# Kernel tuning notes

Hardware: AMD Instinct MI355X
Metric: run time of the kernel (lower is better)

The kernel has to match this reference:

```python
import jax, jax.numpy as jnp
import numpy as np


def setup_inputs() -> dict:
    key = jax.random.key(0)
    k1, k2, k3 = jax.random.split(key, 3)
    b, c, h, w = 4, 64, 64, 64
    content = jax.random.normal(k1, (b, c, h, w), dtype=jnp.float32)
    content_s = jax.random.normal(k2, (b, c, h, w), dtype=jnp.float32)
    style = jax.random.normal(k3, (b, c, h, w), dtype=jnp.float32)
    return {"content": content, "content_s": content_s, "style": style}


def reference(content, content_s, style):
    b, c, h, w = content.shape
    hw = h * w
    Fc = content.reshape(b, c, hw)      # [b, c, HW]
    Fs = content_s.reshape(b, c, hw)    # [b, c, HW]
    Fst = style.reshape(b, c, hw)       # [b, c, HW]
    # S[b, q, k] = sum_c Fc[b, c, q] * Fs[b, c, k]  (Fc transposed as in torch)
    S = jnp.einsum('bcq,bck->bqk', Fc, Fs)
    S = jax.nn.softmax(S, axis=-1)
    # O = style @ S^T : O[b, c, q] = sum_k Fst[b, c, k] * S[b, q, k]
    O = jnp.einsum('bck,bqk->bcq', Fst, S).reshape(b, c, h, w)
    return jnp.concatenate((content, O), axis=1)
```

## Files before the change

kernel.cpp:

```cpp
#include <hip/hip_runtime.h>
#include <math.h>


#define Bb 4
#define Cc 64
#define HWs 4096
#define SPLITS 4
#define TILES_PER_SPLIT 16
#define RLOG2E 1.44269504088896340736f

typedef _Float16 half8 __attribute__((ext_vector_type(8)));
typedef _Float16 half4 __attribute__((ext_vector_type(4)));
typedef float floatx4 __attribute__((ext_vector_type(4)));

__global__ __launch_bounds__(256) void prep_k(const float* __restrict__ content,
                                              const float* __restrict__ Fs,
                                              const float* __restrict__ Fst,
                                              float* __restrict__ out,
                                              _Float16* __restrict__ Kt,
                                              _Float16* __restrict__ Vt) {
    const int bid = blockIdx.x;
    const int t = threadIdx.x;
    if (bid < 1024) {
        int i4 = bid * 256 + t;
        const float4* c4 = (const float4*)content;
        const float4* v4 = (const float4*)Fst;
        float4* o4 = (float4*)out;
        int b = i4 >> 16, rem = i4 & 65535;
        o4[(size_t)b * 131072 + rem] = c4[i4];
        float4 v = v4[i4];
        half4 h;
        h[0] = (_Float16)v.x; h[1] = (_Float16)v.y;
        h[2] = (_Float16)v.z; h[3] = (_Float16)v.w;
        *(half4*)(Vt + (size_t)i4 * 4) = h;
    } else {
        __shared__ _Float16 T[16][72];
        int e = bid - 1024;
        int b = e >> 8;
        int hw0 = (e & 255) * 16;
        const float* sb = Fs + (size_t)b * Cc * HWs;
        {
            int c = t >> 2, x4 = (t & 3) * 4;
            float4 v = *(const float4*)(sb + (size_t)c * HWs + hw0 + x4);
            T[x4 + 0][c] = (_Float16)v.x;
            T[x4 + 1][c] = (_Float16)v.y;
            T[x4 + 2][c] = (_Float16)v.z;
            T[x4 + 3][c] = (_Float16)v.w;
        }
        __syncthreads();
        if (t < 128) {
            int row = t >> 3, g = t & 7;
            _Float16* db = Kt + (size_t)b * HWs * Cc;
            *(half8*)(db + (size_t)(hw0 + row) * Cc + g * 8) = *(half8*)&T[row][g * 8];
        }
    }
}

__global__ __launch_bounds__(256, 2) void attn_k(const float* __restrict__ Fc,
                                                 const _Float16* __restrict__ Kt,
                                                 const _Float16* __restrict__ Vt,
                                                 _Float16* __restrict__ Opart,
                                                 float2* __restrict__ ml) {
    const int tid  = threadIdx.x;
    const int w    = tid >> 6;
    const int lane = tid & 63;
    const int quad = lane >> 4;
    const int l15  = lane & 15;
    const int qg = blockIdx.x & 31;
    const int b  = (blockIdx.x >> 5) & 3;
    const int s  = blockIdx.x >> 7;
    const int k0base = s * TILES_PER_SPLIT * 64;
    const int qA = qg * 128 + w * 32 + l15;
    const int qB = qA + 16;

    __shared__ _Float16 Kl[2][64 * 64];
    __shared__ _Float16 Vl[2][64 * 64];
    __shared__ _Float16 Ps[4][32][72];

    const float*    Fcb = Fc + (size_t)b * Cc * HWs;
    const _Float16* Kb  = Kt + (size_t)b * HWs * Cc;
    const _Float16* Vb  = Vt + (size_t)b * Cc * HWs;

    const bool isK  = tid < 128;
    const int  sl   = tid & 127;
    const int  srow = sl >> 3;
    const int  sjg  = sl & 7;
    const int  ssw  = (sjg ^ (srow & 7)) * 8;

    half8 qf[2][2];
    #pragma unroll
    for (int j = 0; j < 8; ++j) {
        qf[0][0][j] = (_Float16)(Fcb[(size_t)(quad * 8 + j) * HWs + qA] * RLOG2E);
        qf[0][1][j] = (_Float16)(Fcb[(size_t)(32 + quad * 8 + j) * HWs + qA] * RLOG2E);
        qf[1][0][j] = (_Float16)(Fcb[(size_t)(quad * 8 + j) * HWs + qB] * RLOG2E);
        qf[1][1][j] = (_Float16)(Fcb[(size_t)(32 + quad * 8 + j) * HWs + qB] * RLOG2E);
    }

    half8 st[4];
    auto stage_load = [&](int kt) {
        int kk0 = k0base + kt * 64;
        #pragma unroll
        for (int i = 0; i < 4; ++i) {
            int row = srow + 16 * i;
            if (isK) st[i] = *(const half8*)(Kb + (size_t)(kk0 + row) * 64 + sjg * 8);
            else     st[i] = *(const half8*)(Vb + (size_t)row * HWs + kk0 + sjg * 8);
        }
    };
    auto stage_write = [&](int p) {
        #pragma unroll
        for (int i = 0; i < 4; ++i) {
            int row = srow + 16 * i;
            if (isK) *(half8*)&Kl[p][row * 64 + ssw] = st[i];
            else     *(half8*)&Vl[p][row * 64 + ssw] = st[i];
        }
    };

    floatx4 acc[2][4];
    #pragma unroll
    for (int g = 0; g < 2; ++g)
        #pragma unroll
        for (int m = 0; m < 4; ++m) acc[g][m] = (floatx4)(0.0f);
    float m_run[2] = {-INFINITY, -INFINITY};
    float lsum[2] = {0.0f, 0.0f};

    stage_load(0);
    stage_write(0);
    stage_load(1);
    __syncthreads();

    const int swl = (l15 & 7);
    for (int kt = 0; kt < TILES_PER_SPLIT; ++kt) {
        const int p = kt & 1;
        if (kt + 1 < TILES_PER_SPLIT) stage_write(p ^ 1);
        if (kt + 2 < TILES_PER_SPLIT) stage_load(kt + 2);

        half8 ka[4][2];
        #pragma unroll
        for (int m = 0; m < 4; ++m)
            #pragma unroll
            for (int cs = 0; cs < 2; ++cs)
                ka[m][cs] = *(const half8*)&Kl[p][(m * 16 + l15) * 64 + (((cs * 4 + quad) ^ swl) * 8)];

        floatx4 sv[2][4];
        #pragma unroll
        for (int m = 0; m < 4; ++m) {
            #pragma unroll
            for (int g = 0; g < 2; ++g) {
                sv[g][m] = __builtin_amdgcn_mfma_f32_16x16x32_f16(ka[m][0], qf[g][0], (floatx4)(0.0f), 0, 0, 0);
                sv[g][m] = __builtin_amdgcn_mfma_f32_16x16x32_f16(ka[m][1], qf[g][1], sv[g][m], 0, 0, 0);
            }
        }

        half8 va[4][2];
        #pragma unroll
        for (int m = 0; m < 4; ++m)
            #pragma unroll
            for (int ks = 0; ks < 2; ++ks)
                va[m][ks] = *(const half8*)&Vl[p][(m * 16 + l15) * 64 + (((ks * 4 + quad) ^ swl) * 8)];

        half8 pb[2][2];
        #pragma unroll
        for (int g = 0; g < 2; ++g) {
            float mx = -INFINITY;
            #pragma unroll
            for (int m = 0; m < 4; ++m)
                #pragma unroll
                for (int r = 0; r < 4; ++r) mx = fmaxf(mx, sv[g][m][r]);
            mx = fmaxf(mx, __shfl_xor(mx, 16));
            mx = fmaxf(mx, __shfl_xor(mx, 32));
            float m_new = fmaxf(m_run[g], mx);
            float alpha = exp2f(m_run[g] - m_new);
            m_run[g] = m_new;
            float part = 0.0f;
            #pragma unroll
            for (int m = 0; m < 4; ++m)
                #pragma unroll
                for (int r = 0; r < 4; ++r) {
                    float e = exp2f(sv[g][m][r] - m_new);
                    sv[g][m][r] = e;
                    part += e;
                }
            lsum[g] = lsum[g] * alpha + part;
            #pragma unroll
            for (int m = 0; m < 4; ++m)
                #pragma unroll
                for (int r = 0; r < 4; ++r) acc[g][m][r] *= alpha;

            #pragma unroll
            for (int m = 0; m < 4; ++m) {
                half4 pp;
                pp[0] = (_Float16)sv[g][m][0]; pp[1] = (_Float16)sv[g][m][1];
                pp[2] = (_Float16)sv[g][m][2]; pp[3] = (_Float16)sv[g][m][3];
                *(half4*)&Ps[w][g * 16 + l15][m * 16 + quad * 4] = pp;
            }
            pb[g][0] = *(half8*)&Ps[w][g * 16 + l15][quad * 8];
            pb[g][1] = *(half8*)&Ps[w][g * 16 + l15][32 + quad * 8];
        }

        #pragma unroll
        for (int m = 0; m < 4; ++m)
            #pragma unroll
            for (int g = 0; g < 2; ++g) {
                acc[g][m] = __builtin_amdgcn_mfma_f32_16x16x32_f16(va[m][0], pb[g][0], acc[g][m], 0, 0, 0);
                acc[g][m] = __builtin_amdgcn_mfma_f32_16x16x32_f16(va[m][1], pb[g][1], acc[g][m], 0, 0, 0);
            }

        __syncthreads();
    }

    _Float16* op = Opart + (((size_t)s * Bb + b) * Cc) * HWs;
    #pragma unroll
    for (int g = 0; g < 2; ++g) {
        lsum[g] += __shfl_xor(lsum[g], 16);
        lsum[g] += __shfl_xor(lsum[g], 32);
        int q = (g == 0) ? qA : qB;
        #pragma unroll
        for (int m = 0; m < 4; ++m)
            #pragma unroll
            for (int r = 0; r < 4; ++r) {
                int c = m * 16 + quad * 4 + r;
                op[(size_t)c * HWs + q] = (_Float16)acc[g][m][r];
            }
        if (quad == 0)
            ml[((size_t)b * HWs + q) * SPLITS + s] = make_float2(m_run[g], lsum[g]);
    }
}

__global__ __launch_bounds__(256) void combine_k(const _Float16* __restrict__ Opart,
                                                 const float2* __restrict__ ml,
                                                 float* __restrict__ out) {
    int idx = blockIdx.x * 256 + threadIdx.x;
    int q = idx & 4095;
    int c = (idx >> 12) & 63;
    int b = idx >> 18;
    const float2* mlp = ml + ((size_t)b * HWs + q) * SPLITS;
    float2 mls[SPLITS];
    #pragma unroll
    for (int s = 0; s < SPLITS; ++s) mls[s] = mlp[s];
    float M = -INFINITY;
    #pragma unroll
    for (int s = 0; s < SPLITS; ++s) M = fmaxf(M, mls[s].x);
    float l = 0.0f, wgt[SPLITS];
    #pragma unroll
    for (int s = 0; s < SPLITS; ++s) {
        wgt[s] = exp2f(mls[s].x - M);
        l += wgt[s] * mls[s].y;
    }
    float o = 0.0f;
    #pragma unroll
    for (int s = 0; s < SPLITS; ++s)
        o += wgt[s] * (float)Opart[(((size_t)s * Bb + b) * Cc + c) * HWs + q];
    out[((size_t)b * 2 * Cc + Cc + c) * HWs + q] = o / l;
}

extern "C" void kernel_launch(void* const* d_in, const int* in_sizes, int n_in,
                              void* d_out, int out_size, void* d_ws, size_t ws_size,
                              hipStream_t stream) {
    const float* content   = (const float*)d_in[0];
    const float* content_s = (const float*)d_in[1];
    const float* style     = (const float*)d_in[2];
    float* out = (float*)d_out;

    _Float16* Kt = (_Float16*)d_ws;
    _Float16* Vt = Kt + (size_t)Bb * HWs * Cc;
    _Float16* Opart = Vt + (size_t)Bb * Cc * HWs;
    float2*   ml = (float2*)(Opart + (size_t)SPLITS * Bb * Cc * HWs);

    prep_k<<<dim3(2048), dim3(256), 0, stream>>>(content, content_s, style, out, Kt, Vt);
    attn_k<<<dim3(SPLITS * Bb * 32), dim3(256), 0, stream>>>(content, Kt, Vt, Opart, ml);
    combine_k<<<dim3(4096), dim3(256), 0, stream>>>(Opart, ml, out);
}
```

Baseline: 110.1 us.

## Pretranspose Q to fp16, double queries per warp, use more key splits

```diff
diff --git a/kernel.cpp b/kernel.cpp
--- a/kernel.cpp
+++ b/kernel.cpp
@@ -5,8 +5,8 @@
 #define Bb 4
 #define Cc 64
 #define HWs 4096
-#define SPLITS 4
-#define TILES_PER_SPLIT 16
+#define SPLITS 8
+#define TPS 8
 #define RLOG2E 1.44269504088896340736f
 
 typedef _Float16 half8 __attribute__((ext_vector_type(8)));
@@ -14,14 +14,17 @@
 typedef float floatx4 __attribute__((ext_vector_type(4)));
 
 __global__ __launch_bounds__(256) void prep_k(const float* __restrict__ content,
+                                              const float* __restrict__ Fc,
                                               const float* __restrict__ Fs,
                                               const float* __restrict__ Fst,
                                               float* __restrict__ out,
+                                              _Float16* __restrict__ Qt,
                                               _Float16* __restrict__ Kt,
                                               _Float16* __restrict__ Vt) {
     const int bid = blockIdx.x;
     const int t = threadIdx.x;
-    if (bid < 1024) {
+    const int sect = bid >> 10;
+    if (sect == 0) {
         int i4 = bid * 256 + t;
         const float4* c4 = (const float4*)content;
         const float4* v4 = (const float4*)Fst;
@@ -35,28 +38,31 @@
         *(half4*)(Vt + (size_t)i4 * 4) = h;
     } else {
         __shared__ _Float16 T[16][72];
-        int e = bid - 1024;
+        int e = bid & 1023;
         int b = e >> 8;
         int hw0 = (e & 255) * 16;
-        const float* sb = Fs + (size_t)b * Cc * HWs;
+        const float* src = (sect == 1) ? Fs : Fc;
+        _Float16* dst = (sect == 1) ? Kt : Qt;
+        const float scale = (sect == 1) ? 1.0f : RLOG2E;
+        const float* sb = src + (size_t)b * Cc * HWs;
         {
             int c = t >> 2, x4 = (t & 3) * 4;
             float4 v = *(const float4*)(sb + (size_t)c * HWs + hw0 + x4);
-            T[x4 + 0][c] = (_Float16)v.x;
-            T[x4 + 1][c] = (_Float16)v.y;
-            T[x4 + 2][c] = (_Float16)v.z;
-            T[x4 + 3][c] = (_Float16)v.w;
+            T[x4 + 0][c] = (_Float16)(v.x * scale);
+            T[x4 + 1][c] = (_Float16)(v.y * scale);
+            T[x4 + 2][c] = (_Float16)(v.z * scale);
+            T[x4 + 3][c] = (_Float16)(v.w * scale);
         }
         __syncthreads();
         if (t < 128) {
             int row = t >> 3, g = t & 7;
-            _Float16* db = Kt + (size_t)b * HWs * Cc;
+            _Float16* db = dst + (size_t)b * HWs * Cc;
             *(half8*)(db + (size_t)(hw0 + row) * Cc + g * 8) = *(half8*)&T[row][g * 8];
         }
     }
 }
 
-__global__ __launch_bounds__(256, 2) void attn_k(const float* __restrict__ Fc,
+__global__ __launch_bounds__(256, 2) void attn_k(const _Float16* __restrict__ Qt,
                                                  const _Float16* __restrict__ Kt,
                                                  const _Float16* __restrict__ Vt,
                                                  _Float16* __restrict__ Opart,
@@ -66,20 +72,19 @@
     const int lane = tid & 63;
     const int quad = lane >> 4;
     const int l15  = lane & 15;
-    const int qg = blockIdx.x & 31;
-    const int b  = (blockIdx.x >> 5) & 3;
-    const int s  = blockIdx.x >> 7;
-    const int k0base = s * TILES_PER_SPLIT * 64;
-    const int qA = qg * 128 + w * 32 + l15;
-    const int qB = qA + 16;
+    const int qg = blockIdx.x & 15;
+    const int b  = (blockIdx.x >> 4) & 3;
+    const int s  = blockIdx.x >> 6;
+    const int k0base = s * TPS * 64;
+    const int qbase = qg * 256 + w * 64 + l15;
 
     __shared__ _Float16 Kl[2][64 * 64];
     __shared__ _Float16 Vl[2][64 * 64];
-    __shared__ _Float16 Ps[4][32][72];
-
-    const float*    Fcb = Fc + (size_t)b * Cc * HWs;
-    const _Float16* Kb  = Kt + (size_t)b * HWs * Cc;
-    const _Float16* Vb  = Vt + (size_t)b * Cc * HWs;
+    __shared__ _Float16 Ps[4][2][16][72];
+
+    const _Float16* Qb = Qt + (size_t)b * HWs * Cc;
+    const _Float16* Kb = Kt + (size_t)b * HWs * Cc;
+    const _Float16* Vb = Vt + (size_t)b * Cc * HWs;
 
     const bool isK  = tid < 128;
     const int  sl   = tid & 127;
@@ -87,13 +92,11 @@
     const int  sjg  = sl & 7;
     const int  ssw  = (sjg ^ (srow & 7)) * 8;
 
-    half8 qf[2][2];
-    #pragma unroll
-    for (int j = 0; j < 8; ++j) {
-        qf[0][0][j] = (_Float16)(Fcb[(size_t)(quad * 8 + j) * HWs + qA] * RLOG2E);
-        qf[0][1][j] = (_Float16)(Fcb[(size_t)(32 + quad * 8 + j) * HWs + qA] * RLOG2E);
-        qf[1][0][j] = (_Float16)(Fcb[(size_t)(quad * 8 + j) * HWs + qB] * RLOG2E);
-        qf[1][1][j] = (_Float16)(Fcb[(size_t)(32 + quad * 8 + j) * HWs + qB] * RLOG2E);
+    half8 qf[4][2];
+    #pragma unroll
+    for (int g = 0; g < 4; ++g) {
+        qf[g][0] = *(const half8*)(Qb + (size_t)(qbase + g * 16) * Cc + quad * 8);
+        qf[g][1] = *(const half8*)(Qb + (size_t)(qbase + g * 16) * Cc + 32 + quad * 8);
     }
 
     half8 st[4];
@@ -115,13 +118,13 @@
         }
     };
 
-    floatx4 acc[2][4];
-    #pragma unroll
-    for (int g = 0; g < 2; ++g)
+    floatx4 acc[4][4];
+    #pragma unroll
+    for (int g = 0; g < 4; ++g)
         #pragma unroll
         for (int m = 0; m < 4; ++m) acc[g][m] = (floatx4)(0.0f);
-    float m_run[2] = {-INFINITY, -INFINITY};
-    float lsum[2] = {0.0f, 0.0f};
+    float m_run[4] = {-INFINITY, -INFINITY, -INFINITY, -INFINITY};
+    float lsum[4] = {0.0f, 0.0f, 0.0f, 0.0f};
 
     stage_load(0);
     stage_write(0);
@@ -129,25 +132,20 @@
     __syncthreads();
 
     const int swl = (l15 & 7);
-    for (int kt = 0; kt < TILES_PER_SPLIT; ++kt) {
+    for (int kt = 0; kt < TPS; ++kt) {
         const int p = kt & 1;
-        if (kt + 1 < TILES_PER_SPLIT) stage_write(p ^ 1);
-        if (kt + 2 < TILES_PER_SPLIT) stage_load(kt + 2);
-
-        half8 ka[4][2];
-        #pragma unroll
-        for (int m = 0; m < 4; ++m)
-            #pragma unroll
-            for (int cs = 0; cs < 2; ++cs)
-                ka[m][cs] = *(const half8*)&Kl[p][(m * 16 + l15) * 64 + (((cs * 4 + quad) ^ swl) * 8)];
-
-        floatx4 sv[2][4];
+        if (kt + 1 < TPS) stage_write(p ^ 1);
+        if (kt + 2 < TPS) stage_load(kt + 2);
+
+        floatx4 sv[4][4];
         #pragma unroll
         for (int m = 0; m < 4; ++m) {
-            #pragma unroll
-            for (int g = 0; g < 2; ++g) {
-                sv[g][m] = __builtin_amdgcn_mfma_f32_16x16x32_f16(ka[m][0], qf[g][0], (floatx4)(0.0f), 0, 0, 0);
-                sv[g][m] = __builtin_amdgcn_mfma_f32_16x16x32_f16(ka[m][1], qf[g][1], sv[g][m], 0, 0, 0);
+            half8 ka0 = *(const half8*)&Kl[p][(m * 16 + l15) * 64 + ((quad ^ swl) * 8)];
+            half8 ka1 = *(const half8*)&Kl[p][(m * 16 + l15) * 64 + (((4 + quad) ^ swl) * 8)];
+            #pragma unroll
+            for (int g = 0; g < 4; ++g) {
+                sv[g][m] = __builtin_amdgcn_mfma_f32_16x16x32_f16(ka0, qf[g][0], (floatx4)(0.0f), 0, 0, 0);
+                sv[g][m] = __builtin_amdgcn_mfma_f32_16x16x32_f16(ka1, qf[g][1], sv[g][m], 0, 0, 0);
             }
         }
 
@@ -158,9 +156,8 @@
             for (int ks = 0; ks < 2; ++ks)
                 va[m][ks] = *(const half8*)&Vl[p][(m * 16 + l15) * 64 + (((ks * 4 + quad) ^ swl) * 8)];
 
-        half8 pb[2][2];
-        #pragma unroll
-        for (int g = 0; g < 2; ++g) {
+        #pragma unroll
+        for (int g = 0; g < 4; ++g) {
             float mx = -INFINITY;
             #pragma unroll
             for (int m = 0; m < 4; ++m)
@@ -191,29 +188,27 @@
                 half4 pp;
                 pp[0] = (_Float16)sv[g][m][0]; pp[1] = (_Float16)sv[g][m][1];
                 pp[2] = (_Float16)sv[g][m][2]; pp[3] = (_Float16)sv[g][m][3];
-                *(half4*)&Ps[w][g * 16 + l15][m * 16 + quad * 4] = pp;
-            }
-            pb[g][0] = *(half8*)&Ps[w][g * 16 + l15][quad * 8];
-            pb[g][1] = *(half8*)&Ps[w][g * 16 + l15][32 + quad * 8];
-        }
-
-        #pragma unroll
-        for (int m = 0; m < 4; ++m)
-            #pragma unroll
-            for (int g = 0; g < 2; ++g) {
-                acc[g][m] = __builtin_amdgcn_mfma_f32_16x16x32_f16(va[m][0], pb[g][0], acc[g][m], 0, 0, 0);
-                acc[g][m] = __builtin_amdgcn_mfma_f32_16x16x32_f16(va[m][1], pb[g][1], acc[g][m], 0, 0, 0);
-            }
+                *(half4*)&Ps[w][g & 1][l15][m * 16 + quad * 4] = pp;
+            }
+            half8 pb0 = *(half8*)&Ps[w][g & 1][l15][quad * 8];
+            half8 pb1 = *(half8*)&Ps[w][g & 1][l15][32 + quad * 8];
+
+            #pragma unroll
+            for (int m = 0; m < 4; ++m) {
+                acc[g][m] = __builtin_amdgcn_mfma_f32_16x16x32_f16(va[m][0], pb0, acc[g][m], 0, 0, 0);
+                acc[g][m] = __builtin_amdgcn_mfma_f32_16x16x32_f16(va[m][1], pb1, acc[g][m], 0, 0, 0);
+            }
+        }
 
         __syncthreads();
     }
 
     _Float16* op = Opart + (((size_t)s * Bb + b) * Cc) * HWs;
     #pragma unroll
-    for (int g = 0; g < 2; ++g) {
+    for (int g = 0; g < 4; ++g) {
         lsum[g] += __shfl_xor(lsum[g], 16);
         lsum[g] += __shfl_xor(lsum[g], 32);
-        int q = (g == 0) ? qA : qB;
+        int q = qbase + g * 16;
         #pragma unroll
         for (int m = 0; m < 4; ++m)
             #pragma unroll
@@ -261,12 +256,14 @@
     const float* style     = (const float*)d_in[2];
     float* out = (float*)d_out;
 
-    _Float16* Kt = (_Float16*)d_ws;
+    _Float16* Qt = (_Float16*)d_ws;
+    _Float16* Kt = Qt + (size_t)Bb * HWs * Cc;
     _Float16* Vt = Kt + (size_t)Bb * HWs * Cc;
     _Float16* Opart = Vt + (size_t)Bb * Cc * HWs;
     float2*   ml = (float2*)(Opart + (size_t)SPLITS * Bb * Cc * HWs);
 
-    prep_k<<<dim3(2048), dim3(256), 0, stream>>>(content, content_s, style, out, Kt, Vt);
-    attn_k<<<dim3(SPLITS * Bb * 32), dim3(256), 0, stream>>>(content, Kt, Vt, Opart, ml);
+    prep_k<<<dim3(3072), dim3(256), 0, stream>>>(content, content, content_s, style,
+                                                 out, Qt, Kt, Vt);
+    attn_k<<<dim3(SPLITS * Bb * 16), dim3(256), 0, stream>>>(Qt, Kt, Vt, Opart, ml);
     combine_k<<<dim3(4096), dim3(256), 0, stream>>>(Opart, ml, out);
 }
```

New measurement: 117.7 us. 1.07x slower.
